# Performance work log

Measured on AMD Instinct MI355X. Metric: run time of the kernel, lower is better.

## Reference

```python
import jax, jax.numpy as jnp
import numpy as np

MASK_ID = 3
MAX_SEN = 128
SEN_DIM = 128
EMBED = 1024


def setup_inputs() -> dict:
    key = jax.random.key(0)
    ks = jax.random.split(key, 12)
    B, S, E, D = 8, 8192, EMBED, SEN_DIM
    s = 0.02
    return {
        "input_ids": jax.random.randint(ks[0], (B, S), 0, 64),
        "hidden_states": jax.random.normal(ks[1], (B, S, E), jnp.float32),
        "Wv": jax.random.normal(ks[2], (E, D), jnp.float32) * s,
        "bv": jnp.zeros((D,), jnp.float32),
        "Wq": jax.random.normal(ks[3], (E, D), jnp.float32) * s,
        "bq": jnp.zeros((D,), jnp.float32),
        "Wk": jax.random.normal(ks[4], (D, D), jnp.float32) * s,
        "bk": jnp.zeros((D,), jnp.float32),
        "Wvt": jax.random.normal(ks[5], (D, D), jnp.float32) * s,
        "bvt": jnp.zeros((D,), jnp.float32),
        "Wo": jax.random.normal(ks[6], (D, E), jnp.float32) * s,
        "bo": jnp.zeros((E,), jnp.float32),
    }


def reference(input_ids, hidden_states, Wv, bv, Wq, bq, Wk, bk, Wvt, bvt, Wo, bo):
    B, S, E = hidden_states.shape
    dt = hidden_states.dtype

    # sentence segmentation: each mask token t with running count c belongs to bucket c-1
    mask = input_ids == MASK_ID                               # (B, S)
    csum = jnp.cumsum(mask.astype(jnp.int32), axis=1)         # (B, S)
    # tokens that are not mask tokens (or overflow max_sen_num) go to dummy bucket MAX_SEN
    seg = jnp.where(mask & (csum <= MAX_SEN), csum - 1, MAX_SEN)  # (B, S)

    # segment-sum replacement for torch.bmm(sen_pos_mask, hidden_states)
    b_idx = jnp.arange(B)[:, None]
    pooled = jnp.zeros((B, MAX_SEN + 1, E), dt).at[b_idx, seg].add(hidden_states)[:, :MAX_SEN]  # (B, M, E)

    static_sen_states = pooled @ Wv + bv                      # (B, M, 128)

    q_token = (hidden_states @ Wq + bq) * (SEN_DIM ** -0.5)   # (B, S, 128)
    k_sen = static_sen_states @ Wk + bk                       # (B, M, 128)
    v_sen = static_sen_states @ Wvt + bvt                     # (B, M, 128)

    # token t may attend to sentences 0..csum[t]-1
    tmp_mask = (jnp.arange(MAX_SEN)[None, None, :] + 1) <= csum[:, :, None]  # (B, S, M)
    neg = jnp.finfo(dt).min
    logits = jnp.einsum('bsd,bmd->bsm', q_token, k_sen) + jnp.where(tmp_mask, jnp.zeros((), dt), neg)
    attn = jax.nn.softmax(logits, axis=-1) * tmp_mask.astype(dt)  # (B, S, M)

    sen_attn_output = jnp.einsum('bsm,bmd->bsd', attn, v_sen) @ Wo + bo  # (B, S, E)
    return sen_attn_output
```

## Files before the change

### kernel.cpp

```cpp
#include <hip/hip_runtime.h>
#include <hip/hip_bf16.h>

#define MASK_ID 3
#define MAX_SEN 128
#define NB 8
#define SEQ 8192
#define EMB 1024
#define DIM 128
#define TS 32

typedef __attribute__((ext_vector_type(8))) short short8v;
typedef __attribute__((ext_vector_type(4))) float f32x4;

#define MFMA(a, b, c) __builtin_amdgcn_mfma_f32_16x16x32_bf16(a, b, c, 0, 0, 0)

__device__ __forceinline__ short f2b(float x) {
    union { float f; unsigned u; } v; v.f = x;
    unsigned r = (v.u + 0x7FFFu + ((v.u >> 16) & 1u)) >> 16;
    return (short)r;
}

__global__ __launch_bounds__(1024) void seg_kernel(const int* __restrict__ ids,
                                                   int* __restrict__ pos,
                                                   int* __restrict__ nvis) {
    int b = blockIdx.x;
    int tid = threadIdx.x;
    __shared__ int sc[1024];
    __shared__ int sc2[1024];
    const int PER = SEQ / 1024;
    int base = b * SEQ + tid * PER;

    int ids_l[PER];
    int cnt = 0;
    #pragma unroll
    for (int j = 0; j < PER; j++) {
        ids_l[j] = ids[base + j];
        cnt += (ids_l[j] == MASK_ID) ? 1 : 0;
    }
    if (tid < MAX_SEN) pos[b * MAX_SEN + tid] = -1;
    sc[tid] = cnt;
    __syncthreads();

    int* src = sc;
    int* dst = sc2;
    for (int off = 1; off < 1024; off <<= 1) {
        int v = src[tid];
        if (tid >= off) v += src[tid - off];
        dst[tid] = v;
        __syncthreads();
        int* t = src; src = dst; dst = t;
    }
    int incl = src[tid];
    int run = incl - cnt;

    #pragma unroll
    for (int j = 0; j < PER; j++) {
        if (ids_l[j] == MASK_ID) {
            run++;
            if (run <= MAX_SEN) pos[b * MAX_SEN + run - 1] = tid * PER + j;
        }
        int nv = run; if (nv > MAX_SEN) nv = MAX_SEN;
        nvis[base + j] = nv;
    }
}

__global__ __launch_bounds__(256) void prep_w(const float* __restrict__ Wq,
                                              const float* __restrict__ Wo,
                                              short* __restrict__ WqT,
                                              short* __restrict__ WoT) {
    int idx = blockIdx.x * 256 + threadIdx.x;
    int d = idx >> 10, e = idx & 1023;
    WqT[idx] = f2b(Wq[e * DIM + d]);
    int e2 = idx >> 7, d2 = idx & 127;
    WoT[idx] = f2b(Wo[d2 * EMB + e2]);
}

__global__ __launch_bounds__(128) void statkv_kernel(const float* __restrict__ hidden,
                                                     const float* __restrict__ Wv, const float* __restrict__ bv,
                                                     const float* __restrict__ Wk, const float* __restrict__ bk,
                                                     const float* __restrict__ Wvt, const float* __restrict__ bvt,
                                                     const int* __restrict__ pos,
                                                     short* __restrict__ k_bf, short* __restrict__ vT_bf) {
    int m = blockIdx.x, b = blockIdx.y;
    int d = threadIdx.x;
    __shared__ float h[EMB];
    __shared__ float srow[DIM];
    int p = pos[b * MAX_SEN + m];
    float acc = bv[d];
    if (p >= 0) {
        const float* hp = hidden + ((size_t)b * SEQ + p) * EMB;
        for (int e = d; e < EMB; e += 128) h[e] = hp[e];
        __syncthreads();
        for (int e = 0; e < EMB; e++) acc += h[e] * Wv[e * DIM + d];
    }
    srow[d] = acc;
    __syncthreads();
    float ka = bk[d], va = bvt[d];
    for (int e = 0; e < DIM; e++) {
        float sv = srow[e];
        ka += sv * Wk[e * DIM + d];
        va += sv * Wvt[e * DIM + d];
    }
    k_bf[((size_t)b * MAX_SEN + m) * DIM + d] = f2b(ka);
    vT_bf[((size_t)b * DIM + d) * MAX_SEN + m] = f2b(va);
}

__global__ __launch_bounds__(256, 4) void attn_kernel(
    const float* __restrict__ hidden,
    const short* __restrict__ WqT, const float* __restrict__ bq,
    const short* __restrict__ k_bf, const short* __restrict__ vT_bf,
    const short* __restrict__ WoT, const float* __restrict__ bo,
    const int* __restrict__ nvis,
    float* __restrict__ out) {
    int blk = blockIdx.x;
    int b  = blk >> 8;
    int s0 = (blk & 255) * TS;
    int tid = threadIdx.x;
    int lane = tid & 63;
    int w  = tid >> 6;
    int lr = lane & 15;
    int lq = lane >> 4;

    __shared__ char uAbuf[32 * 132 * 4];
    __shared__ short qP[32 * 128];
    __shared__ short odB[32 * 128];

    char* hAc = uAbuf;
    float* lg = (float*)uAbuf;
    char* qPc = (char*)qP;
    char* odc = (char*)odB;

    const size_t hrow = (size_t)b * SEQ + s0;
    f32x4 zero = {0.f, 0.f, 0.f, 0.f};

    float4 pf[8];
    #pragma unroll
    for (int g = 0; g < 4; g++) {
        int G = tid + g * 256;
        int t = G >> 5, e8 = (G & 31) << 3;
        const float* hp = hidden + (hrow + t) * EMB + e8;
        pf[2 * g]     = *(const float4*)hp;
        pf[2 * g + 1] = *(const float4*)(hp + 4);
    }

    f32x4 a00 = zero, a01 = zero, a10 = zero, a11 = zero;
    for (int ec = 0; ec < 4; ec++) {
        __syncthreads();
        #pragma unroll
        for (int g = 0; g < 4; g++) {
            int G = tid + g * 256;
            int t = G >> 5, e8 = (G & 31) << 3;
            short8v hh;
            hh[0] = f2b(pf[2 * g].x); hh[1] = f2b(pf[2 * g].y);
            hh[2] = f2b(pf[2 * g].z); hh[3] = f2b(pf[2 * g].w);
            hh[4] = f2b(pf[2 * g + 1].x); hh[5] = f2b(pf[2 * g + 1].y);
            hh[6] = f2b(pf[2 * g + 1].z); hh[7] = f2b(pf[2 * g + 1].w);
            int byte = (t * 512 + e8 * 2) ^ ((t & 7) << 4);
            *(short8v*)(hAc + byte) = hh;
        }
        if (ec < 3) {
            #pragma unroll
            for (int g = 0; g < 4; g++) {
                int G = tid + g * 256;
                int t = G >> 5, e8 = (G & 31) << 3;
                const float* hp = hidden + (hrow + t) * EMB + (ec + 1) * 256 + e8;
                pf[2 * g]     = *(const float4*)hp;
                pf[2 * g + 1] = *(const float4*)(hp + 4);
            }
        }
        __syncthreads();
        const short* bp0 = WqT + (w * 32 + lr) * 1024 + ec * 256 + lq * 8;
        const short* bp1 = bp0 + 16 * 1024;
        #pragma unroll
        for (int kk = 0; kk < 8; kk++) {
            short8v fa0 = *(short8v*)(hAc + ((lr * 512 + kk * 64 + lq * 16) ^ ((lr & 7) << 4)));
            short8v fa1 = *(short8v*)(hAc + (((16 + lr) * 512 + kk * 64 + lq * 16) ^ ((lr & 7) << 4)));
            short8v fb0 = *(const short8v*)(bp0 + kk * 32);
            short8v fb1 = *(const short8v*)(bp1 + kk * 32);
            a00 = MFMA(fa0, fb0, a00); a01 = MFMA(fa0, fb1, a01);
            a10 = MFMA(fa1, fb0, a10); a11 = MFMA(fa1, fb1, a11);
        }
    }
    {
        const float scale = 0.08838834764831845f;
        int d0 = w * 32 + lr;
        float bq0 = bq[d0], bq1 = bq[d0 + 16];
        #pragma unroll
        for (int r = 0; r < 4; r++) {
            int r0 = lq * 4 + r, r1 = 16 + r0;
            *(short*)(qPc + ((r0 * 256 + d0 * 2) ^ ((r0 & 7) << 4)))        = f2b((a00[r] + bq0) * scale);
            *(short*)(qPc + ((r0 * 256 + (d0 + 16) * 2) ^ ((r0 & 7) << 4))) = f2b((a01[r] + bq1) * scale);
            *(short*)(qPc + ((r1 * 256 + d0 * 2) ^ ((r1 & 7) << 4)))        = f2b((a10[r] + bq0) * scale);
            *(short*)(qPc + ((r1 * 256 + (d0 + 16) * 2) ^ ((r1 & 7) << 4))) = f2b((a11[r] + bq1) * scale);
        }
    }
    __syncthreads();

    {
        f32x4 l00 = zero, l01 = zero, l10 = zero, l11 = zero;
        const short* kbp0 = k_bf + ((size_t)b << 14) + (w * 32 + lr) * 128 + lq * 8;
        const short* kbp1 = kbp0 + 16 * 128;
        #pragma unroll
        for (int kk = 0; kk < 4; kk++) {
            short8v fa0 = *(short8v*)(qPc + ((lr * 256 + kk * 64 + lq * 16) ^ ((lr & 7) << 4)));
            short8v fa1 = *(short8v*)(qPc + (((16 + lr) * 256 + kk * 64 + lq * 16) ^ ((lr & 7) << 4)));
            short8v fb0 = *(const short8v*)(kbp0 + kk * 32);
            short8v fb1 = *(const short8v*)(kbp1 + kk * 32);
            l00 = MFMA(fa0, fb0, l00); l01 = MFMA(fa0, fb1, l01);
            l10 = MFMA(fa1, fb0, l10); l11 = MFMA(fa1, fb1, l11);
        }
        int m0 = w * 32 + lr;
        #pragma unroll
        for (int r = 0; r < 4; r++) {
            int r0 = lq * 4 + r, r1 = 16 + r0;
            lg[r0 * 132 + m0]      = l00[r];
            lg[r0 * 132 + m0 + 16] = l01[r];
            lg[r1 * 132 + m0]      = l10[r];
            lg[r1 * 132 + m0 + 16] = l11[r];
        }
    }
    __syncthreads();

    {
        int t = tid >> 3, sub = tid & 7;
        int nv = nvis[b * SEQ + s0 + t];
        float pv[16];
        float mx = -3.0e38f;
        #pragma unroll
        for (int i = 0; i < 16; i++) {
            int m = sub * 16 + i;
            float vv = lg[t * 132 + m];
            pv[i] = vv;
            if (m < nv) mx = fmaxf(mx, vv);
        }
        mx = fmaxf(mx, __shfl_xor(mx, 1));
        mx = fmaxf(mx, __shfl_xor(mx, 2));
        mx = fmaxf(mx, __shfl_xor(mx, 4));
        float sum = 0.f;
        #pragma unroll
        for (int i = 0; i < 16; i++) {
            int m = sub * 16 + i;
            float e = (m < nv) ? __expf(pv[i] - mx) : 0.f;
            pv[i] = e;
            sum += e;
        }
        sum += __shfl_xor(sum, 1);
        sum += __shfl_xor(sum, 2);
        sum += __shfl_xor(sum, 4);
        float inv = (nv > 0) ? 1.0f / sum : 0.f;
        #pragma unroll
        for (int i = 0; i < 16; i++) {
            int m = sub * 16 + i;
            *(short*)(qPc + ((t * 256 + m * 2) ^ ((t & 7) << 4))) = f2b(pv[i] * inv);
        }
    }
    __syncthreads();

    {
        f32x4 o00 = zero, o01 = zero, o10 = zero, o11 = zero;
        const short* vbp0 = vT_bf + ((size_t)b << 14) + (w * 32 + lr) * 128 + lq * 8;
        const short* vbp1 = vbp0 + 16 * 128;
        #pragma unroll
        for (int kk = 0; kk < 4; kk++) {
            short8v fa0 = *(short8v*)(qPc + ((lr * 256 + kk * 64 + lq * 16) ^ ((lr & 7) << 4)));
            short8v fa1 = *(short8v*)(qPc + (((16 + lr) * 256 + kk * 64 + lq * 16) ^ ((lr & 7) << 4)));
            short8v fb0 = *(const short8v*)(vbp0 + kk * 32);
            short8v fb1 = *(const short8v*)(vbp1 + kk * 32);
            o00 = MFMA(fa0, fb0, o00); o01 = MFMA(fa0, fb1, o01);
            o10 = MFMA(fa1, fb0, o10); o11 = MFMA(fa1, fb1, o11);
        }
        int d0 = w * 32 + lr;
        #pragma unroll
        for (int r = 0; r < 4; r++) {
            int r0 = lq * 4 + r, r1 = 16 + r0;
            *(short*)(odc + ((r0 * 256 + d0 * 2) ^ ((r0 & 7) << 4)))        = f2b(o00[r]);
            *(short*)(odc + ((r0 * 256 + (d0 + 16) * 2) ^ ((r0 & 7) << 4))) = f2b(o01[r]);
            *(short*)(odc + ((r1 * 256 + d0 * 2) ^ ((r1 & 7) << 4)))        = f2b(o10[r]);
            *(short*)(odc + ((r1 * 256 + (d0 + 16) * 2) ^ ((r1 & 7) << 4))) = f2b(o11[r]);
        }
    }
    __syncthreads();

    {
        short8v af0[4], af1[4];
        #pragma unroll
        for (int kk = 0; kk < 4; kk++) {
            af0[kk] = *(short8v*)(odc + ((lr * 256 + kk * 64 + lq * 16) ^ ((lr & 7) << 4)));
            af1[kk] = *(short8v*)(odc + (((16 + lr) * 256 + kk * 64 + lq * 16) ^ ((lr & 7) << 4)));
        }
        #pragma unroll
        for (int pass = 0; pass < 4; pass++) {
            int ep = w * 256 + pass * 64;
            f32x4 ac0[4], ac1[4];
            #pragma unroll
            for (int e2 = 0; e2 < 4; e2++) { ac0[e2] = zero; ac1[e2] = zero; }
            #pragma unroll
            for (int kk = 0; kk < 4; kk++) {
                #pragma unroll
                for (int e2 = 0; e2 < 4; e2++) {
                    const short8v bb = *(const short8v*)(WoT + (ep + e2 * 16 + lr) * 128 + kk * 32 + lq * 8);
                    ac0[e2] = MFMA(af0[kk], bb, ac0[e2]);
                    ac1[e2] = MFMA(af1[kk], bb, ac1[e2]);
                }
            }
            #pragma unroll
            for (int e2 = 0; e2 < 4; e2++) {
                int col = ep + e2 * 16 + lr;
                float bov = bo[col];
                #pragma unroll
                for (int r = 0; r < 4; r++) {
                    out[(hrow + lq * 4 + r) * EMB + col]      = ac0[e2][r] + bov;
                    out[(hrow + 16 + lq * 4 + r) * EMB + col] = ac1[e2][r] + bov;
                }
            }
        }
    }
}

extern "C" void kernel_launch(void* const* d_in, const int* in_sizes, int n_in,
                              void* d_out, int out_size, void* d_ws, size_t ws_size,
                              hipStream_t stream) {
    const int*   ids    = (const int*)d_in[0];
    const float* hidden = (const float*)d_in[1];
    const float* Wv     = (const float*)d_in[2];
    const float* bv     = (const float*)d_in[3];
    const float* Wq     = (const float*)d_in[4];
    const float* bq     = (const float*)d_in[5];
    const float* Wk     = (const float*)d_in[6];
    const float* bk     = (const float*)d_in[7];
    const float* Wvt    = (const float*)d_in[8];
    const float* bvt    = (const float*)d_in[9];
    const float* Wo     = (const float*)d_in[10];
    const float* bo     = (const float*)d_in[11];

    char* ws = (char*)d_ws;
    int*   pos   = (int*)ws;
    int*   nvis  = (int*)(ws + (4 << 10));
    short* k_bf  = (short*)(ws + (260 << 10));
    short* vT_bf = (short*)(ws + (516 << 10));
    short* WqT   = (short*)(ws + (772 << 10));
    short* WoT   = (short*)(ws + (1028 << 10));

    seg_kernel<<<NB, 1024, 0, stream>>>(ids, pos, nvis);
    prep_w<<<512, 256, 0, stream>>>(Wq, Wo, WqT, WoT);
    dim3 g2(MAX_SEN, NB);
    statkv_kernel<<<g2, 128, 0, stream>>>(hidden, Wv, bv, Wk, bk, Wvt, bvt, pos, k_bf, vT_bf);
    attn_kernel<<<NB * (SEQ / TS), 256, 0, stream>>>(hidden, WqT, bq, k_bf, vT_bf, WoT, bo,
                                                     nvis, (float*)d_out);
}
```

Measured before the change: 243.6 us.

## Split fused attention into Q-projection and attention/output kernels with 64-row tiles

The single fused attention kernel becomes two kernels. The first projects hidden states to a bf16 Q buffer in workspace. The second does logits, softmax, PV and the Wo projection over 64-token tiles, and its softmax loops only over the visible sentence count instead of all 128 slots. Larger tiles give more reuse of the weight fragments per MFMA. The cost is an extra global round trip for Q (about 16 MB of bf16), an extra launch, and lower occupancy in the attention kernel because of its larger shared-memory footprint.

```diff
diff --git a/kernel.cpp b/kernel.cpp
--- a/kernel.cpp
+++ b/kernel.cpp
@@ -7,9 +7,9 @@
 #define SEQ 8192
 #define EMB 1024
 #define DIM 128
-#define TS 32
 
 typedef __attribute__((ext_vector_type(8))) short short8v;
+typedef __attribute__((ext_vector_type(4))) short short4v;
 typedef __attribute__((ext_vector_type(4))) float f32x4;
 
 #define MFMA(a, b, c) __builtin_amdgcn_mfma_f32_16x16x32_bf16(a, b, c, 0, 0, 0)
@@ -105,213 +105,214 @@
     vT_bf[((size_t)b * DIM + d) * MAX_SEN + m] = f2b(va);
 }
 
-__global__ __launch_bounds__(256, 4) void attn_kernel(
-    const float* __restrict__ hidden,
-    const short* __restrict__ WqT, const float* __restrict__ bq,
-    const short* __restrict__ k_bf, const short* __restrict__ vT_bf,
-    const short* __restrict__ WoT, const float* __restrict__ bo,
-    const int* __restrict__ nvis,
-    float* __restrict__ out) {
+__global__ __launch_bounds__(256, 4) void q_kernel(const float* __restrict__ hidden,
+                                                   const short* __restrict__ WqT,
+                                                   const float* __restrict__ bq,
+                                                   short* __restrict__ q_bf) {
     int blk = blockIdx.x;
-    int b  = blk >> 8;
-    int s0 = (blk & 255) * TS;
+    size_t r0 = (size_t)blk * 64;
     int tid = threadIdx.x;
-    int lane = tid & 63;
-    int w  = tid >> 6;
-    int lr = lane & 15;
-    int lq = lane >> 4;
-
-    __shared__ char uAbuf[32 * 132 * 4];
-    __shared__ short qP[32 * 128];
-    __shared__ short odB[32 * 128];
-
-    char* hAc = uAbuf;
-    float* lg = (float*)uAbuf;
-    char* qPc = (char*)qP;
+    int lane = tid & 63, w = tid >> 6, lr = lane & 15, lq = lane >> 4;
+
+    __shared__ char hAc[64 * 256];
+
+    f32x4 acc[4][2];
+    #pragma unroll
+    for (int rg = 0; rg < 4; rg++)
+        #pragma unroll
+        for (int cf = 0; cf < 2; cf++) acc[rg][cf] = {0.f, 0.f, 0.f, 0.f};
+
+    float4 pf[8];
+    #pragma unroll
+    for (int g = 0; g < 8; g++) {
+        int G = g * 256 + tid;
+        int row = G >> 5, e4 = (G & 31) << 2;
+        pf[g] = *(const float4*)(hidden + (r0 + row) * EMB + e4);
+    }
+
+    for (int c = 0; c < 8; c++) {
+        __syncthreads();
+        #pragma unroll
+        for (int g = 0; g < 8; g++) {
+            int G = g * 256 + tid;
+            int row = G >> 5, e4 = (G & 31) << 2;
+            short4v hh;
+            hh[0] = f2b(pf[g].x); hh[1] = f2b(pf[g].y);
+            hh[2] = f2b(pf[g].z); hh[3] = f2b(pf[g].w);
+            int byte = (row * 256 + e4 * 2) ^ ((row & 7) << 4);
+            *(short4v*)(hAc + byte) = hh;
+        }
+        if (c < 7) {
+            #pragma unroll
+            for (int g = 0; g < 8; g++) {
+                int G = g * 256 + tid;
+                int row = G >> 5, e4 = (G & 31) << 2;
+                pf[g] = *(const float4*)(hidden + (r0 + row) * EMB + (c + 1) * 128 + e4);
+            }
+        }
+        __syncthreads();
+        #pragma unroll
+        for (int kk = 0; kk < 4; kk++) {
+            short8v fa[4];
+            #pragma unroll
+            for (int rg = 0; rg < 4; rg++)
+                fa[rg] = *(short8v*)(hAc + (((rg * 16 + lr) * 256 + kk * 64 + lq * 16) ^ ((lr & 7) << 4)));
+            #pragma unroll
+            for (int cf = 0; cf < 2; cf++) {
+                const short8v fb = *(const short8v*)(WqT + (size_t)(w * 32 + cf * 16 + lr) * 1024
+                                                     + c * 128 + kk * 32 + lq * 8);
+                #pragma unroll
+                for (int rg = 0; rg < 4; rg++) acc[rg][cf] = MFMA(fa[rg], fb, acc[rg][cf]);
+            }
+        }
+    }
+    const float scale = 0.08838834764831845f;
+    #pragma unroll
+    for (int cf = 0; cf < 2; cf++) {
+        int col = w * 32 + cf * 16 + lr;
+        float bqv = bq[col];
+        #pragma unroll
+        for (int rg = 0; rg < 4; rg++)
+            #pragma unroll
+            for (int r = 0; r < 4; r++)
+                q_bf[(r0 + rg * 16 + lq * 4 + r) * 128 + col] = f2b((acc[rg][cf][r] + bqv) * scale);
+    }
+}
+
+__global__ __launch_bounds__(256, 2) void atto_kernel(const short* __restrict__ q_bf,
+                                                      const short* __restrict__ k_bf,
+                                                      const short* __restrict__ vT_bf,
+                                                      const short* __restrict__ WoT,
+                                                      const float* __restrict__ bo,
+                                                      const int* __restrict__ nvis,
+                                                      float* __restrict__ out) {
+    int blk = blockIdx.x;
+    int b = blk >> 7;
+    int sl = (blk & 127) * 64;
+    size_t s0 = (size_t)b * SEQ + sl;
+    int tid = threadIdx.x;
+    int lane = tid & 63, w = tid >> 6, lr = lane & 15, lq = lane >> 4;
+
+    __shared__ float lg[64 * 132];
+    __shared__ short pP[64 * 128];
+    __shared__ short odB[64 * 128];
+    char* pPc = (char*)pP;
     char* odc = (char*)odB;
 
-    const size_t hrow = (size_t)b * SEQ + s0;
-    f32x4 zero = {0.f, 0.f, 0.f, 0.f};
-
-    float4 pf[8];
-    #pragma unroll
-    for (int g = 0; g < 4; g++) {
-        int G = tid + g * 256;
-        int t = G >> 5, e8 = (G & 31) << 3;
-        const float* hp = hidden + (hrow + t) * EMB + e8;
-        pf[2 * g]     = *(const float4*)hp;
-        pf[2 * g + 1] = *(const float4*)(hp + 4);
-    }
-
-    f32x4 a00 = zero, a01 = zero, a10 = zero, a11 = zero;
-    for (int ec = 0; ec < 4; ec++) {
-        __syncthreads();
-        #pragma unroll
-        for (int g = 0; g < 4; g++) {
-            int G = tid + g * 256;
-            int t = G >> 5, e8 = (G & 31) << 3;
-            short8v hh;
-            hh[0] = f2b(pf[2 * g].x); hh[1] = f2b(pf[2 * g].y);
-            hh[2] = f2b(pf[2 * g].z); hh[3] = f2b(pf[2 * g].w);
-            hh[4] = f2b(pf[2 * g + 1].x); hh[5] = f2b(pf[2 * g + 1].y);
-            hh[6] = f2b(pf[2 * g + 1].z); hh[7] = f2b(pf[2 * g + 1].w);
-            int byte = (t * 512 + e8 * 2) ^ ((t & 7) << 4);
-            *(short8v*)(hAc + byte) = hh;
-        }
-        if (ec < 3) {
-            #pragma unroll
-            for (int g = 0; g < 4; g++) {
-                int G = tid + g * 256;
-                int t = G >> 5, e8 = (G & 31) << 3;
-                const float* hp = hidden + (hrow + t) * EMB + (ec + 1) * 256 + e8;
-                pf[2 * g]     = *(const float4*)hp;
-                pf[2 * g + 1] = *(const float4*)(hp + 4);
-            }
-        }
-        __syncthreads();
-        const short* bp0 = WqT + (w * 32 + lr) * 1024 + ec * 256 + lq * 8;
-        const short* bp1 = bp0 + 16 * 1024;
-        #pragma unroll
-        for (int kk = 0; kk < 8; kk++) {
-            short8v fa0 = *(short8v*)(hAc + ((lr * 512 + kk * 64 + lq * 16) ^ ((lr & 7) << 4)));
-            short8v fa1 = *(short8v*)(hAc + (((16 + lr) * 512 + kk * 64 + lq * 16) ^ ((lr & 7) << 4)));
-            short8v fb0 = *(const short8v*)(bp0 + kk * 32);
-            short8v fb1 = *(const short8v*)(bp1 + kk * 32);
-            a00 = MFMA(fa0, fb0, a00); a01 = MFMA(fa0, fb1, a01);
-            a10 = MFMA(fa1, fb0, a10); a11 = MFMA(fa1, fb1, a11);
-        }
-    }
     {
-        const float scale = 0.08838834764831845f;
-        int d0 = w * 32 + lr;
-        float bq0 = bq[d0], bq1 = bq[d0 + 16];
-        #pragma unroll
-        for (int r = 0; r < 4; r++) {
-            int r0 = lq * 4 + r, r1 = 16 + r0;
-            *(short*)(qPc + ((r0 * 256 + d0 * 2) ^ ((r0 & 7) << 4)))        = f2b((a00[r] + bq0) * scale);
-            *(short*)(qPc + ((r0 * 256 + (d0 + 16) * 2) ^ ((r0 & 7) << 4))) = f2b((a01[r] + bq1) * scale);
-            *(short*)(qPc + ((r1 * 256 + d0 * 2) ^ ((r1 & 7) << 4)))        = f2b((a10[r] + bq0) * scale);
-            *(short*)(qPc + ((r1 * 256 + (d0 + 16) * 2) ^ ((r1 & 7) << 4))) = f2b((a11[r] + bq1) * scale);
-        }
+        f32x4 acc[4][2];
+        #pragma unroll
+        for (int rg = 0; rg < 4; rg++)
+            #pragma unroll
+            for (int mf = 0; mf < 2; mf++) acc[rg][mf] = {0.f, 0.f, 0.f, 0.f};
+        #pragma unroll
+        for (int kk = 0; kk < 4; kk++) {
+            short8v fa[4];
+            #pragma unroll
+            for (int rg = 0; rg < 4; rg++)
+                fa[rg] = *(const short8v*)(q_bf + (s0 + rg * 16 + lr) * 128 + kk * 32 + lq * 8);
+            #pragma unroll
+            for (int mf = 0; mf < 2; mf++) {
+                const short8v fb = *(const short8v*)(k_bf + ((size_t)b << 14)
+                                                     + (w * 32 + mf * 16 + lr) * 128 + kk * 32 + lq * 8);
+                #pragma unroll
+                for (int rg = 0; rg < 4; rg++) acc[rg][mf] = MFMA(fa[rg], fb, acc[rg][mf]);
+            }
+        }
+        #pragma unroll
+        for (int rg = 0; rg < 4; rg++)
+            #pragma unroll
+            for (int mf = 0; mf < 2; mf++)
+                #pragma unroll
+                for (int r = 0; r < 4; r++)
+                    lg[(rg * 16 + lq * 4 + r) * 132 + w * 32 + mf * 16 + lr] = acc[rg][mf][r];
     }
     __syncthreads();
 
     {
-        f32x4 l00 = zero, l01 = zero, l10 = zero, l11 = zero;
-        const short* kbp0 = k_bf + ((size_t)b << 14) + (w * 32 + lr) * 128 + lq * 8;
-        const short* kbp1 = kbp0 + 16 * 128;
-        #pragma unroll
-        for (int kk = 0; kk < 4; kk++) {
-            short8v fa0 = *(short8v*)(qPc + ((lr * 256 + kk * 64 + lq * 16) ^ ((lr & 7) << 4)));
-            short8v fa1 = *(short8v*)(qPc + (((16 + lr) * 256 + kk * 64 + lq * 16) ^ ((lr & 7) << 4)));
-            short8v fb0 = *(const short8v*)(kbp0 + kk * 32);
-            short8v fb1 = *(const short8v*)(kbp1 + kk * 32);
-            l00 = MFMA(fa0, fb0, l00); l01 = MFMA(fa0, fb1, l01);
-            l10 = MFMA(fa1, fb0, l10); l11 = MFMA(fa1, fb1, l11);
-        }
-        int m0 = w * 32 + lr;
-        #pragma unroll
-        for (int r = 0; r < 4; r++) {
-            int r0 = lq * 4 + r, r1 = 16 + r0;
-            lg[r0 * 132 + m0]      = l00[r];
-            lg[r0 * 132 + m0 + 16] = l01[r];
-            lg[r1 * 132 + m0]      = l10[r];
-            lg[r1 * 132 + m0 + 16] = l11[r];
-        }
-    }
-    __syncthreads();
-
-    {
-        int t = tid >> 3, sub = tid & 7;
-        int nv = nvis[b * SEQ + s0 + t];
-        float pv[16];
+        int t = tid >> 2, sub = tid & 3;
+        int nv = nvis[s0 + t];
+        const float* lrow = lg + t * 132 + sub * 32;
+        int cnt = nv - sub * 32;
+        if (cnt < 0) cnt = 0; if (cnt > 32) cnt = 32;
         float mx = -3.0e38f;
-        #pragma unroll
-        for (int i = 0; i < 16; i++) {
-            int m = sub * 16 + i;
-            float vv = lg[t * 132 + m];
-            pv[i] = vv;
-            if (m < nv) mx = fmaxf(mx, vv);
-        }
+        for (int i = 0; i < cnt; i++) mx = fmaxf(mx, lrow[i]);
         mx = fmaxf(mx, __shfl_xor(mx, 1));
         mx = fmaxf(mx, __shfl_xor(mx, 2));
-        mx = fmaxf(mx, __shfl_xor(mx, 4));
         float sum = 0.f;
-        #pragma unroll
-        for (int i = 0; i < 16; i++) {
-            int m = sub * 16 + i;
-            float e = (m < nv) ? __expf(pv[i] - mx) : 0.f;
-            pv[i] = e;
-            sum += e;
-        }
+        for (int i = 0; i < cnt; i++) sum += __expf(lrow[i] - mx);
         sum += __shfl_xor(sum, 1);
         sum += __shfl_xor(sum, 2);
-        sum += __shfl_xor(sum, 4);
         float inv = (nv > 0) ? 1.0f / sum : 0.f;
-        #pragma unroll
-        for (int i = 0; i < 16; i++) {
-            int m = sub * 16 + i;
-            *(short*)(qPc + ((t * 256 + m * 2) ^ ((t & 7) << 4))) = f2b(pv[i] * inv);
+        #pragma unroll 8
+        for (int i = 0; i < 32; i++) {
+            int m = sub * 32 + i;
+            float e = (i < cnt) ? __expf(lrow[i] - mx) * inv : 0.f;
+            *(short*)(pPc + ((t * 256 + m * 2) ^ ((t & 7) << 4))) = f2b(e);
         }
     }
     __syncthreads();
 
     {
-        f32x4 o00 = zero, o01 = zero, o10 = zero, o11 = zero;
-        const short* vbp0 = vT_bf + ((size_t)b << 14) + (w * 32 + lr) * 128 + lq * 8;
-        const short* vbp1 = vbp0 + 16 * 128;
+        f32x4 acc[4][2];
+        #pragma unroll
+        for (int rg = 0; rg < 4; rg++)
+            #pragma unroll
+            for (int df = 0; df < 2; df++) acc[rg][df] = {0.f, 0.f, 0.f, 0.f};
         #pragma unroll
         for (int kk = 0; kk < 4; kk++) {
-            short8v fa0 = *(short8v*)(qPc + ((lr * 256 + kk * 64 + lq * 16) ^ ((lr & 7) << 4)));
-            short8v fa1 = *(short8v*)(qPc + (((16 + lr) * 256 + kk * 64 + lq * 16) ^ ((lr & 7) << 4)));
-            short8v fb0 = *(const short8v*)(vbp0 + kk * 32);
-            short8v fb1 = *(const short8v*)(vbp1 + kk * 32);
-            o00 = MFMA(fa0, fb0, o00); o01 = MFMA(fa0, fb1, o01);
-            o10 = MFMA(fa1, fb0, o10); o11 = MFMA(fa1, fb1, o11);
-        }
-        int d0 = w * 32 + lr;
-        #pragma unroll
-        for (int r = 0; r < 4; r++) {
-            int r0 = lq * 4 + r, r1 = 16 + r0;
-            *(short*)(odc + ((r0 * 256 + d0 * 2) ^ ((r0 & 7) << 4)))        = f2b(o00[r]);
-            *(short*)(odc + ((r0 * 256 + (d0 + 16) * 2) ^ ((r0 & 7) << 4))) = f2b(o01[r]);
-            *(short*)(odc + ((r1 * 256 + d0 * 2) ^ ((r1 & 7) << 4)))        = f2b(o10[r]);
-            *(short*)(odc + ((r1 * 256 + (d0 + 16) * 2) ^ ((r1 & 7) << 4))) = f2b(o11[r]);
-        }
+            short8v fa[4];
+            #pragma unroll
+            for (int rg = 0; rg < 4; rg++)
+                fa[rg] = *(short8v*)(pPc + (((rg * 16 + lr) * 256 + kk * 64 + lq * 16) ^ ((lr & 7) << 4)));
+            #pragma unroll
+            for (int df = 0; df < 2; df++) {
+                const short8v fb = *(const short8v*)(vT_bf + ((size_t)b << 14)
+                                                     + (w * 32 + df * 16 + lr) * 128 + kk * 32 + lq * 8);
+                #pragma unroll
+                for (int rg = 0; rg < 4; rg++) acc[rg][df] = MFMA(fa[rg], fb, acc[rg][df]);
+            }
+        }
+        #pragma unroll
+        for (int rg = 0; rg < 4; rg++)
+            #pragma unroll
+            for (int df = 0; df < 2; df++)
+                #pragma unroll
+                for (int r = 0; r < 4; r++) {
+                    int row = rg * 16 + lq * 4 + r;
+                    int col = w * 32 + df * 16 + lr;
+                    *(short*)(odc + ((row * 256 + col * 2) ^ ((row & 7) << 4))) = f2b(acc[rg][df][r]);
+                }
     }
     __syncthreads();
 
     {
-        short8v af0[4], af1[4];
-        #pragma unroll
-        for (int kk = 0; kk < 4; kk++) {
-            af0[kk] = *(short8v*)(odc + ((lr * 256 + kk * 64 + lq * 16) ^ ((lr & 7) << 4)));
-            af1[kk] = *(short8v*)(odc + (((16 + lr) * 256 + kk * 64 + lq * 16) ^ ((lr & 7) << 4)));
-        }
+        short8v af[4];
+        #pragma unroll
+        for (int kk = 0; kk < 4; kk++)
+            af[kk] = *(short8v*)(odc + (((w * 16 + lr) * 256 + kk * 64 + lq * 16) ^ ((lr & 7) << 4)));
         #pragma unroll
         for (int pass = 0; pass < 4; pass++) {
-            int ep = w * 256 + pass * 64;
-            f32x4 ac0[4], ac1[4];
-            #pragma unroll
-            for (int e2 = 0; e2 < 4; e2++) { ac0[e2] = zero; ac1[e2] = zero; }
+            int ep = pass * 256;
+            f32x4 ac[16];
+            #pragma unroll
+            for (int e2 = 0; e2 < 16; e2++) ac[e2] = {0.f, 0.f, 0.f, 0.f};
             #pragma unroll
             for (int kk = 0; kk < 4; kk++) {
                 #pragma unroll
-                for (int e2 = 0; e2 < 4; e2++) {
-                    const short8v bb = *(const short8v*)(WoT + (ep + e2 * 16 + lr) * 128 + kk * 32 + lq * 8);
-                    ac0[e2] = MFMA(af0[kk], bb, ac0[e2]);
-                    ac1[e2] = MFMA(af1[kk], bb, ac1[e2]);
+                for (int e2 = 0; e2 < 16; e2++) {
+                    const short8v bb = *(const short8v*)(WoT + (size_t)(ep + e2 * 16 + lr) * 128
+                                                         + kk * 32 + lq * 8);
+                    ac[e2] = MFMA(af[kk], bb, ac[e2]);
                 }
             }
             #pragma unroll
-            for (int e2 = 0; e2 < 4; e2++) {
+            for (int e2 = 0; e2 < 16; e2++) {
                 int col = ep + e2 * 16 + lr;
                 float bov = bo[col];
                 #pragma unroll
-                for (int r = 0; r < 4; r++) {
-                    out[(hrow + lq * 4 + r) * EMB + col]      = ac0[e2][r] + bov;
-                    out[(hrow + 16 + lq * 4 + r) * EMB + col] = ac1[e2][r] + bov;
-                }
+                for (int r = 0; r < 4; r++)
+                    out[(s0 + w * 16 + lq * 4 + r) * EMB + col] = ac[e2][r] + bov;
             }
         }
     }
@@ -340,11 +341,13 @@
     short* vT_bf = (short*)(ws + (516 << 10));
     short* WqT   = (short*)(ws + (772 << 10));
     short* WoT   = (short*)(ws + (1028 << 10));
+    short* q_bf  = (short*)(ws + (1284 << 10));
 
     seg_kernel<<<NB, 1024, 0, stream>>>(ids, pos, nvis);
     prep_w<<<512, 256, 0, stream>>>(Wq, Wo, WqT, WoT);
     dim3 g2(MAX_SEN, NB);
     statkv_kernel<<<g2, 128, 0, stream>>>(hidden, Wv, bv, Wk, bk, Wvt, bvt, pos, k_bf, vT_bf);
-    attn_kernel<<<NB * (SEQ / TS), 256, 0, stream>>>(hidden, WqT, bq, k_bf, vT_bf, WoT, bo,
-                                                     nvis, (float*)d_out);
-}
+    q_kernel<<<NB * SEQ / 64, 256, 0, stream>>>(hidden, WqT, bq, q_bf);
+    atto_kernel<<<NB * SEQ / 64, 256, 0, stream>>>(q_bf, k_bf, vT_bf, WoT, bo, nvis,
+                                                   (float*)d_out);
+}
```

Result: slower. 307.2 us (+26.1%).

## Load hidden states directly into MFMA fragments and drop LDS staging for Q projection

Applied to the files above, without the earlier changes.

The Q projection in the attention kernel no longer stages bf16-converted hidden tiles through shared memory with barriers. Each lane now reads its fp32 hidden fragment straight from global memory, converts it and feeds the MFMA. Shared memory is merged into one aliased buffer, softmax uses vector LDS reads and 16-byte probability stores, and the statkv dot loops get multiple accumulators. This removes LDS round-trips and syncs and may raise occupancy, but every wave of a block now fetches the same hidden rows redundantly and with a less coalesced pattern.

```diff
diff --git a/kernel.cpp b/kernel.cpp
--- a/kernel.cpp
+++ b/kernel.cpp
@@ -7,7 +7,6 @@
 #define SEQ 8192
 #define EMB 1024
 #define DIM 128
-#define TS 32
 
 typedef __attribute__((ext_vector_type(8))) short short8v;
 typedef __attribute__((ext_vector_type(4))) float f32x4;
@@ -18,6 +17,13 @@
     union { float f; unsigned u; } v; v.f = x;
     unsigned r = (v.u + 0x7FFFu + ((v.u >> 16) & 1u)) >> 16;
     return (short)r;
+}
+
+__device__ __forceinline__ short8v cvt8(float4 a, float4 b) {
+    short8v r;
+    r[0] = f2b(a.x); r[1] = f2b(a.y); r[2] = f2b(a.z); r[3] = f2b(a.w);
+    r[4] = f2b(b.x); r[5] = f2b(b.y); r[6] = f2b(b.z); r[7] = f2b(b.w);
+    return r;
 }
 
 __global__ __launch_bounds__(1024) void seg_kernel(const int* __restrict__ ids,
@@ -91,18 +97,27 @@
         const float* hp = hidden + ((size_t)b * SEQ + p) * EMB;
         for (int e = d; e < EMB; e += 128) h[e] = hp[e];
         __syncthreads();
-        for (int e = 0; e < EMB; e++) acc += h[e] * Wv[e * DIM + d];
+        float a0 = 0.f, a1 = 0.f, a2 = 0.f, a3 = 0.f;
+        for (int e = 0; e < EMB; e += 4) {
+            a0 += h[e]     * Wv[e * DIM + d];
+            a1 += h[e + 1] * Wv[(e + 1) * DIM + d];
+            a2 += h[e + 2] * Wv[(e + 2) * DIM + d];
+            a3 += h[e + 3] * Wv[(e + 3) * DIM + d];
+        }
+        acc += (a0 + a1) + (a2 + a3);
     }
     srow[d] = acc;
     __syncthreads();
-    float ka = bk[d], va = bvt[d];
-    for (int e = 0; e < DIM; e++) {
-        float sv = srow[e];
-        ka += sv * Wk[e * DIM + d];
-        va += sv * Wvt[e * DIM + d];
-    }
-    k_bf[((size_t)b * MAX_SEN + m) * DIM + d] = f2b(ka);
-    vT_bf[((size_t)b * DIM + d) * MAX_SEN + m] = f2b(va);
+    float k0 = 0.f, k1 = 0.f, v0 = 0.f, v1 = 0.f;
+    for (int e = 0; e < DIM; e += 2) {
+        float s0 = srow[e], s1 = srow[e + 1];
+        k0 += s0 * Wk[e * DIM + d];
+        k1 += s1 * Wk[(e + 1) * DIM + d];
+        v0 += s0 * Wvt[e * DIM + d];
+        v1 += s1 * Wvt[(e + 1) * DIM + d];
+    }
+    k_bf[((size_t)b * MAX_SEN + m) * DIM + d] = f2b(bk[d] + k0 + k1);
+    vT_bf[((size_t)b * DIM + d) * MAX_SEN + m] = f2b(bvt[d] + v0 + v1);
 }
 
 __global__ __launch_bounds__(256, 4) void attn_kernel(
@@ -114,71 +129,45 @@
     float* __restrict__ out) {
     int blk = blockIdx.x;
     int b  = blk >> 8;
-    int s0 = (blk & 255) * TS;
+    int s0 = (blk & 255) * 32;
     int tid = threadIdx.x;
     int lane = tid & 63;
     int w  = tid >> 6;
     int lr = lane & 15;
     int lq = lane >> 4;
 
-    __shared__ char uAbuf[32 * 132 * 4];
-    __shared__ short qP[32 * 128];
-    __shared__ short odB[32 * 128];
-
-    char* hAc = uAbuf;
-    float* lg = (float*)uAbuf;
-    char* qPc = (char*)qP;
-    char* odc = (char*)odB;
+    __shared__ __align__(16) char SH[25088];
+    float* lg  = (float*)SH;
+    char*  pPc = SH;
+    char*  odc = SH + 8448;
+    char*  qPc = SH + 16896;
 
     const size_t hrow = (size_t)b * SEQ + s0;
+    const float* hbase = hidden + hrow * EMB;
     f32x4 zero = {0.f, 0.f, 0.f, 0.f};
 
-    float4 pf[8];
-    #pragma unroll
-    for (int g = 0; g < 4; g++) {
-        int G = tid + g * 256;
-        int t = G >> 5, e8 = (G & 31) << 3;
-        const float* hp = hidden + (hrow + t) * EMB + e8;
-        pf[2 * g]     = *(const float4*)hp;
-        pf[2 * g + 1] = *(const float4*)(hp + 4);
-    }
-
     f32x4 a00 = zero, a01 = zero, a10 = zero, a11 = zero;
-    for (int ec = 0; ec < 4; ec++) {
-        __syncthreads();
-        #pragma unroll
-        for (int g = 0; g < 4; g++) {
-            int G = tid + g * 256;
-            int t = G >> 5, e8 = (G & 31) << 3;
-            short8v hh;
-            hh[0] = f2b(pf[2 * g].x); hh[1] = f2b(pf[2 * g].y);
-            hh[2] = f2b(pf[2 * g].z); hh[3] = f2b(pf[2 * g].w);
-            hh[4] = f2b(pf[2 * g + 1].x); hh[5] = f2b(pf[2 * g + 1].y);
-            hh[6] = f2b(pf[2 * g + 1].z); hh[7] = f2b(pf[2 * g + 1].w);
-            int byte = (t * 512 + e8 * 2) ^ ((t & 7) << 4);
-            *(short8v*)(hAc + byte) = hh;
-        }
-        if (ec < 3) {
+    {
+        const short* wq0 = WqT + (size_t)(w * 32 + lr) * 1024 + lq * 8;
+        const short* wq1 = wq0 + 16 * 1024;
+        const float* h0 = hbase + (size_t)lr * EMB + lq * 8;
+        const float* h1 = h0 + 16 * EMB;
+        #pragma unroll 2
+        for (int c = 0; c < 8; c++) {
             #pragma unroll
-            for (int g = 0; g < 4; g++) {
-                int G = tid + g * 256;
-                int t = G >> 5, e8 = (G & 31) << 3;
-                const float* hp = hidden + (hrow + t) * EMB + (ec + 1) * 256 + e8;
-                pf[2 * g]     = *(const float4*)hp;
-                pf[2 * g + 1] = *(const float4*)(hp + 4);
+            for (int kk = 0; kk < 4; kk++) {
+                int off = c * 128 + kk * 32;
+                float4 x0 = *(const float4*)(h0 + off);
+                float4 x1 = *(const float4*)(h0 + off + 4);
+                float4 y0 = *(const float4*)(h1 + off);
+                float4 y1 = *(const float4*)(h1 + off + 4);
+                short8v fa0 = cvt8(x0, x1);
+                short8v fa1 = cvt8(y0, y1);
+                const short8v fb0 = *(const short8v*)(wq0 + off);
+                const short8v fb1 = *(const short8v*)(wq1 + off);
+                a00 = MFMA(fa0, fb0, a00); a01 = MFMA(fa0, fb1, a01);
+                a10 = MFMA(fa1, fb0, a10); a11 = MFMA(fa1, fb1, a11);
             }
-        }
-        __syncthreads();
-        const short* bp0 = WqT + (w * 32 + lr) * 1024 + ec * 256 + lq * 8;
-        const short* bp1 = bp0 + 16 * 1024;
-        #pragma unroll
-        for (int kk = 0; kk < 8; kk++) {
-            short8v fa0 = *(short8v*)(hAc + ((lr * 512 + kk * 64 + lq * 16) ^ ((lr & 7) << 4)));
-            short8v fa1 = *(short8v*)(hAc + (((16 + lr) * 512 + kk * 64 + lq * 16) ^ ((lr & 7) << 4)));
-            short8v fb0 = *(const short8v*)(bp0 + kk * 32);
-            short8v fb1 = *(const short8v*)(bp1 + kk * 32);
-            a00 = MFMA(fa0, fb0, a00); a01 = MFMA(fa0, fb1, a01);
-            a10 = MFMA(fa1, fb0, a10); a11 = MFMA(fa1, fb1, a11);
         }
     }
     {
@@ -224,23 +213,30 @@
     {
         int t = tid >> 3, sub = tid & 7;
         int nv = nvis[b * SEQ + s0 + t];
+        const float* lrow = lg + t * 132 + sub * 16;
         float pv[16];
+        {
+            float4 v0 = *(const float4*)(lrow + 0);
+            float4 v1 = *(const float4*)(lrow + 4);
+            float4 v2 = *(const float4*)(lrow + 8);
+            float4 v3 = *(const float4*)(lrow + 12);
+            pv[0] = v0.x; pv[1] = v0.y; pv[2]  = v0.z; pv[3]  = v0.w;
+            pv[4] = v1.x; pv[5] = v1.y; pv[6]  = v1.z; pv[7]  = v1.w;
+            pv[8] = v2.x; pv[9] = v2.y; pv[10] = v2.z; pv[11] = v2.w;
+            pv[12] = v3.x; pv[13] = v3.y; pv[14] = v3.z; pv[15] = v3.w;
+        }
+        int base_m = sub * 16;
         float mx = -3.0e38f;
         #pragma unroll
-        for (int i = 0; i < 16; i++) {
-            int m = sub * 16 + i;
-            float vv = lg[t * 132 + m];
-            pv[i] = vv;
-            if (m < nv) mx = fmaxf(mx, vv);
-        }
+        for (int i = 0; i < 16; i++)
+            mx = (base_m + i < nv) ? fmaxf(mx, pv[i]) : mx;
         mx = fmaxf(mx, __shfl_xor(mx, 1));
         mx = fmaxf(mx, __shfl_xor(mx, 2));
         mx = fmaxf(mx, __shfl_xor(mx, 4));
         float sum = 0.f;
         #pragma unroll
         for (int i = 0; i < 16; i++) {
-            int m = sub * 16 + i;
-            float e = (m < nv) ? __expf(pv[i] - mx) : 0.f;
+            float e = (base_m + i < nv) ? __expf(pv[i] - mx) : 0.f;
             pv[i] = e;
             sum += e;
         }
@@ -248,11 +244,16 @@
         sum += __shfl_xor(sum, 2);
         sum += __shfl_xor(sum, 4);
         float inv = (nv > 0) ? 1.0f / sum : 0.f;
-        #pragma unroll
-        for (int i = 0; i < 16; i++) {
-            int m = sub * 16 + i;
-            *(short*)(qPc + ((t * 256 + m * 2) ^ ((t & 7) << 4))) = f2b(pv[i] * inv);
-        }
+
+        __syncthreads();
+
+        short8v p0, p1;
+        #pragma unroll
+        for (int i = 0; i < 8; i++) { p0[i] = f2b(pv[i] * inv); p1[i] = f2b(pv[8 + i] * inv); }
+        int base = t * 256 + sub * 32;
+        int x = (t & 7) << 4;
+        *(short8v*)(pPc + (base ^ x))        = p0;
+        *(short8v*)(pPc + ((base + 16) ^ x)) = p1;
     }
     __syncthreads();
 
@@ -262,8 +263,8 @@
         const short* vbp1 = vbp0 + 16 * 128;
         #pragma unroll
         for (int kk = 0; kk < 4; kk++) {
-            short8v fa0 = *(short8v*)(qPc + ((lr * 256 + kk * 64 + lq * 16) ^ ((lr & 7) << 4)));
-            short8v fa1 = *(short8v*)(qPc + (((16 + lr) * 256 + kk * 64 + lq * 16) ^ ((lr & 7) << 4)));
+            short8v fa0 = *(short8v*)(pPc + ((lr * 256 + kk * 64 + lq * 16) ^ ((lr & 7) << 4)));
+            short8v fa1 = *(short8v*)(pPc + (((16 + lr) * 256 + kk * 64 + lq * 16) ^ ((lr & 7) << 4)));
             short8v fb0 = *(const short8v*)(vbp0 + kk * 32);
             short8v fb1 = *(const short8v*)(vbp1 + kk * 32);
             o00 = MFMA(fa0, fb0, o00); o01 = MFMA(fa0, fb1, o01);
@@ -298,7 +299,8 @@
             for (int kk = 0; kk < 4; kk++) {
                 #pragma unroll
                 for (int e2 = 0; e2 < 4; e2++) {
-                    const short8v bb = *(const short8v*)(WoT + (ep + e2 * 16 + lr) * 128 + kk * 32 + lq * 8);
+                    const short8v bb = *(const short8v*)(WoT + (size_t)(ep + e2 * 16 + lr) * 128
+                                                         + kk * 32 + lq * 8);
                     ac0[e2] = MFMA(af0[kk], bb, ac0[e2]);
                     ac1[e2] = MFMA(af1[kk], bb, ac1[e2]);
                 }
@@ -345,6 +347,6 @@
     prep_w<<<512, 256, 0, stream>>>(Wq, Wo, WqT, WoT);
     dim3 g2(MAX_SEN, NB);
     statkv_kernel<<<g2, 128, 0, stream>>>(hidden, Wv, bv, Wk, bk, Wvt, bvt, pos, k_bf, vT_bf);
-    attn_kernel<<<NB * (SEQ / TS), 256, 0, stream>>>(hidden, WqT, bq, k_bf, vT_bf, WoT, bo,
+    attn_kernel<<<NB * (SEQ / 32), 256, 0, stream>>>(hidden, WqT, bq, k_bf, vT_bf, WoT, bo,
                                                      nvis, (float*)d_out);
 }
```

New measurement: 353.3 us. +45.0%, slower.
